# Kernel optimization log

Hardware: AMD Instinct MI355X
Metric: run time of the kernel (lower is better)

The kernel has to match this reference:

```python
import jax, jax.numpy as jnp
import numpy as np

GRID = 16
PAD = 32
RADIUS = 8
SIGMA = 1.5
B = 8192
N_SEEDS = 24


def setup_inputs() -> dict:
    key = jax.random.key(0)
    k1, k2 = jax.random.split(key)
    # predicted seeds: (x, y, phase), coords in [0, GRID)
    output = jax.random.uniform(k1, (B, N_SEEDS * 3), dtype=jnp.float32) * GRID
    # target seeds: (x, y, amp), coords in [0, 2*GRID)
    targets = jax.random.uniform(k2, (B, N_SEEDS * 3), dtype=jnp.float32) * (2 * GRID)
    return {"output": output, "targets": targets}


def _forward(output, targets):
    Bn = output.shape[0]
    seeds = output.reshape(Bn, -1, 3)   # (B, N, 3): x, y, phase
    tgt = targets.reshape(Bn, -1, 3)    # (B, M, 3): x, y, amp

    # --- discrete Voronoi on GRID x GRID (vectorized over batch) ---
    c = jnp.arange(GRID, dtype=output.dtype)
    xx, yy = jnp.meshgrid(c, c, indexing='ij')  # (GRID, GRID)
    dist = jnp.sqrt((xx[None, :, :, None] - seeds[:, None, None, :, 0]) ** 2
                    + (yy[None, :, :, None] - seeds[:, None, None, :, 1]) ** 2)
    labels = jnp.argmin(dist, axis=-1)  # (B, GRID, GRID) int

    # circular support on the inner grid (np.ogrid[-r:r, -r:r] convention)
    cc = jnp.arange(-RADIUS, RADIUS)
    inner = (cc[:, None] ** 2 + cc[None, :] ** 2) <= RADIUS ** 2
    labels = jnp.where(inner[None], labels, 0)

    # zero-pad voronoi labels to PAD x PAD
    pw = (PAD - GRID) // 2
    padded = jnp.pad(labels, ((0, 0), (pw, pw), (pw, pw)))  # (B, PAD, PAD)

    # --- gather phase per pixel, zero outside circle on padded grid ---
    phases = seeds[:, :, 2]  # (B, N)
    phase = jnp.take_along_axis(phases, padded.reshape(Bn, -1), axis=1).reshape(Bn, PAD, PAD)
    pc = jnp.arange(PAD)
    center = PAD // 2
    outside = (pc[:, None] - center) ** 2 + (pc[None, :] - center) ** 2 > RADIUS ** 2
    phase = jnp.where(outside[None], jnp.zeros_like(phase), phase)

    # --- density = amp(=1) * exp(i * 2*pi * phase), shifted FFT magnitude ---
    two_pi = 2.0 * jnp.pi
    density = jax.lax.complex(jnp.cos(two_pi * phase), jnp.sin(two_pi * phase))
    pred = jnp.fft.fftshift(density, axes=(-2, -1))
    pred = jnp.fft.fft2(pred)
    pred_dp = jnp.abs(jnp.fft.fftshift(pred, axes=(-2, -1)))  # (B, PAD, PAD)

    # --- target diffraction: sum of Gaussians on (2*GRID)x(2*GRID) grid ---
    xc = jnp.arange(PAD, dtype=targets.dtype)  # height == width == 2*GRID == PAD
    tx = tgt[:, :, 0][:, :, None, None]
    ty = tgt[:, :, 1][:, :, None, None]
    amp = tgt[:, :, 2][:, :, None, None]
    # torch: x varies along last axis, y along second-to-last
    d2 = (xc[None, None, None, :] - tx) ** 2 + (xc[None, None, :, None] - ty) ** 2
    tgt_dp = jnp.sum(amp * jnp.exp(-d2 / (2.0 * SIGMA ** 2)), axis=1)  # (B, PAD, PAD)

    # --- chi-square (global max-normalization and reductions) ---
    p = pred_dp / jnp.max(pred_dp)
    t = tgt_dp / jnp.max(tgt_dp)
    return jnp.sum((p - t) ** 2) / jnp.sqrt(jnp.sum(p ** 2) * jnp.sum(t ** 2))


def reference(output, targets):
    return _forward(output, targets)
```

## Files before the change

kernel.cpp:

```cpp
#include <hip/hip_runtime.h>
#include <math.h>

#define NS 24

typedef float v2f __attribute__((ext_vector_type(2)));
typedef float v4f __attribute__((ext_vector_type(4)));


struct PixTab { unsigned short v[196]; };
__device__ constexpr PixTab make_pix() {
    PixTab t{};
    int n = 0;
    const int w[16] = {0,3,5,6,6,7,7,7,8,7,7,7,6,6,5,3};
    for (int yy = 0; yy < 16; ++yy)
        for (int x = 16 - w[yy]; x <= 16 + w[yy]; ++x)
            if (x < 24) { t.v[n] = (unsigned short)((yy << 8) | x); n = n + 1; }
    t.v[195] = (unsigned short)((8 << 8) | 24);
    return t;
}
__device__ constexpr PixTab PIX = make_pix();

struct ZTab { unsigned short v[76]; };
__device__ constexpr ZTab make_ztab() {
    ZTab z{};
    bool mark[16][17] = {};
    const int w[16] = {0,3,5,6,6,7,7,7,8,7,7,7,6,6,5,3};
    for (int yy = 0; yy < 16; ++yy)
        for (int x = 16 - w[yy]; x <= 16 + w[yy]; ++x)
            if (x < 24) mark[yy][x - 8] = true;
    mark[8][16] = true;
    int n = 0;
    for (int yy = 0; yy < 16; ++yy)
        for (int xi = 0; xi < 17; ++xi)
            if (!mark[yy][xi]) { z.v[n] = (unsigned short)(yy * 18 + xi); n = n + 1; }
    return z;
}
__device__ constexpr ZTab ZT = make_ztab();

constexpr float twc_(int p) {
    const float C[17] = {
        1.0f, 0.98078528040323044913f, 0.92387953251128675613f, 0.83146961230254523708f,
        0.70710678118654752440f, 0.55557023301960222474f, 0.38268343236508977173f,
        0.19509032201612826785f, 0.0f,
        -0.19509032201612826785f, -0.38268343236508977173f, -0.55557023301960222474f,
        -0.70710678118654752440f, -0.83146961230254523708f, -0.92387953251128675613f,
        -0.98078528040323044913f, -1.0f };
    return (p <= 16) ? C[p] : C[32 - p];
}
constexpr float tws_(int p) {
    const float S[17] = {
        0.0f, 0.19509032201612826785f, 0.38268343236508977173f, 0.55557023301960222474f,
        0.70710678118654752440f, 0.83146961230254523708f, 0.92387953251128675613f,
        0.98078528040323044913f, 1.0f,
        0.98078528040323044913f, 0.92387953251128675613f, 0.83146961230254523708f,
        0.70710678118654752440f, 0.55557023301960222474f, 0.38268343236508977173f,
        0.19509032201612826785f, 0.0f };
    return (p <= 16) ? -S[p] : S[32 - p];
}
struct alignas(16) TW1T { float v[8 * 18 * 2]; };
__device__ constexpr TW1T make_tw1() {
    TW1T t{};
    for (int l0 = 0; l0 < 8; ++l0)
        for (int xi = 0; xi < 17; ++xi) {
            int p = (l0 * (xi + 8)) & 31;
            t.v[(l0 * 18 + xi) * 2 + 0] = twc_(p);
            t.v[(l0 * 18 + xi) * 2 + 1] = tws_(p);
        }
    return t;
}
__device__ constexpr TW1T TW1G = make_tw1();
struct alignas(16) TW2T { float v[4 * 18 * 2]; };
__device__ constexpr TW2T make_tw2() {
    TW2T t{};
    for (int k0 = 0; k0 < 4; ++k0)
        for (int yp = 0; yp < 16; ++yp) {
            int p = (k0 * (yp + 8)) & 31;
            t.v[(k0 * 18 + yp) * 2 + 0] = twc_(p);
            t.v[(k0 * 18 + yp) * 2 + 1] = tws_(p);
        }
    return t;
}
__device__ constexpr TW2T TW2G = make_tw2();

static __device__ __forceinline__ v2f cmul(v2f e, v2f w) {
    v2f m = (v2f){e.y, e.y} * (v2f){w.y, w.x};
    return __builtin_elementwise_fma((v2f){e.x, e.x}, w, (v2f){-m.x, m.y});
}
static __device__ __forceinline__ float mag(v2f h) {
    v2f q = h * h;
    return sqrtf(q.x + q.y);
}

template <int CTRL>
static __device__ __forceinline__ float dpp_step(float x) {
    int y = __builtin_amdgcn_update_dpp(0, __float_as_int(x), CTRL, 0xf, 0xf, true);
    return __int_as_float(y);
}
static __device__ __forceinline__ float wave_sum(float x) {
    x += dpp_step<0x111>(x);
    x += dpp_step<0x112>(x);
    x += dpp_step<0x114>(x);
    x += dpp_step<0x118>(x);
    x += dpp_step<0x142>(x);
    x += dpp_step<0x143>(x);
    return x;
}
static __device__ __forceinline__ float wave_max(float x) {
    x = fmaxf(x, dpp_step<0x111>(x));
    x = fmaxf(x, dpp_step<0x112>(x));
    x = fmaxf(x, dpp_step<0x114>(x));
    x = fmaxf(x, dpp_step<0x118>(x));
    x = fmaxf(x, dpp_step<0x142>(x));
    x = fmaxf(x, dpp_step<0x143>(x));
    return x;
}

__global__ __launch_bounds__(256)
void loss_main(const float* __restrict__ output, const float* __restrict__ targets,
               float* __restrict__ partials, int B) {
    __shared__ float2 e24s;
    __shared__ __align__(16) float gx[NS * 32];
    __shared__ __align__(16) float gyT[32 * 24];
    __shared__ __align__(16) float e2f[16 * 18 * 2];
    __shared__ __align__(16) float tw2f[4 * 36];
    __shared__ __align__(16) float gT2f[32 * 36];
    __shared__ __align__(16) char uA[5120];
    __shared__ float redm[2][5];

    float* tw1f = (float*)uA;
    float* pmf  = (float*)uA;

    const int b = blockIdx.x;
    const int t = threadIdx.x;
    const float* so = output + b * NS * 3;
    const float* tg = targets + b * NS * 3;

    if (t == 0) {
        float sv0, cv0;
        __sincosf(6.2831853071795864f * so[2], &sv0, &cv0);
        e24s = make_float2(cv0 - 1.0f, sv0);
    }
    if (t < 108) {
        if (t < 72) *(v4f*)&tw1f[t * 4] = *(const v4f*)&TW1G.v[t * 4];
        else        *(v4f*)&tw2f[(t - 72) * 4] = *(const v4f*)&TW2G.v[(t - 72) * 4];
    }
    for (int idx = t; idx < NS * 32; idx += 256) {
        int s = idx >> 5, c = idx & 31;
        float dx = (float)c - tg[3 * s];
        gx[idx] = tg[3 * s + 2] * __expf(dx * dx * (-1.0f / 4.5f));
    }
    for (int idx = t; idx < 32 * 24; idx += 256) {
        int r = idx / 24, s = idx - r * 24;
        float dy = (float)r - tg[3 * s + 1];
        gyT[idx] = __expf(dy * dy * (-1.0f / 4.5f));
    }
    if (t < 98) {
        int pv0 = PIX.v[t], pv1 = PIX.v[t + 98];
        int yy0 = pv0 >> 8, x0 = (pv0 & 255) - 8;
        int yy1 = pv1 >> 8, x1 = (pv1 & 255) - 8;
        v2f FI = {(float)yy0, (float)yy1};
        v2f FJ = {(float)x0, (float)x1};
        v2f bd = {1e30f, 1e30f};
        v2f bph = {0.f, 0.f};
#pragma unroll
        for (int s = 0; s < NS; ++s) {
            float sx = so[3 * s], sy = so[3 * s + 1], phs = so[3 * s + 2];
            v2f dX = FI - (v2f){sx, sx};
            v2f dY = FJ - (v2f){sy, sy};
            v2f d2 = __builtin_elementwise_fma(dX, dX, dY * dY);
            if (d2.x < bd.x) { bd.x = d2.x; bph.x = phs; }
            if (d2.y < bd.y) { bd.y = d2.y; bph.y = phs; }
        }
        float ph1 = (t == 97) ? so[2] : bph.y;
        float sv0, cv0, sv1, cv1;
        __sincosf(6.2831853071795864f * bph.x, &sv0, &cv0);
        __sincosf(6.2831853071795864f * ph1, &sv1, &cv1);
        *(v2f*)&e2f[(yy0 * 18 + x0) * 2] = (v2f){cv0 - 1.0f, sv0};
        *(v2f*)&e2f[(yy1 * 18 + x1) * 2] = (v2f){cv1 - 1.0f, sv1};
    } else if (t < 98 + 76) {
        int idx = (int)ZT.v[t - 98];
        *(v2f*)&e2f[idx * 2] = (v2f){0.f, 0.f};
    }
    __syncthreads();

    v2f ta01 = {0,0}, ta23 = {0,0}, tb01 = {0,0}, tb23 = {0,0};

    if (t < 128) {
        int yy = t >> 3, l0 = t & 7;
        const float* row = &e2f[yy * 36];
        const float* twr = &tw1f[l0 * 36];
        v2f c0 = {0,0}, c1 = {0,0}, c2 = {0,0}, c3 = {0,0};
#pragma unroll
        for (int q = 0; q < 8; ++q) {
            v4f e4 = *(const v4f*)&row[q * 4];
            v4f w4 = *(const v4f*)&twr[q * 4];
            v2f ca = cmul((v2f){e4.x, e4.y}, (v2f){w4.x, w4.y});
            v2f cb = cmul((v2f){e4.z, e4.w}, (v2f){w4.z, w4.w});
            if ((q & 1) == 0) { c0 += ca; c1 += cb; }
            else              { c2 += ca; c3 += cb; }
        }
        {
            v2f e16 = *(const v2f*)&row[32];
            v2f w16 = *(const v2f*)&twr[32];
            c0 += cmul(e16, w16);
        }
        v2f a = c0 + c2, bb = c0 - c2;
        v2f cc = c1 + c3, d = c1 - c3;
        v2f du = {d.y, -d.x};
        *(v2f*)&gT2f[l0 * 36 + yy * 2]        = a + cc;
        *(v2f*)&gT2f[(l0 + 8) * 36 + yy * 2]  = bb + du;
        *(v2f*)&gT2f[(l0 + 16) * 36 + yy * 2] = a - cc;
        *(v2f*)&gT2f[(l0 + 24) * 36 + yy * 2] = bb - du;
    } else {
        int tid2 = t - 128;
        int r = tid2 >> 3;
        int c0i = (tid2 & 7) * 4;
#pragma unroll
        for (int q = 0; q < 6; ++q) {
            v4f gy4a = *(const v4f*)&gyT[r * 24 + q * 4];
            v4f gy4b = *(const v4f*)&gyT[(r + 16) * 24 + q * 4];
#pragma unroll
            for (int j = 0; j < 4; ++j) {
                v4f g4 = *(const v4f*)&gx[(4 * q + j) * 32 + c0i];
                float ga = (j == 0) ? gy4a.x : (j == 1) ? gy4a.y : (j == 2) ? gy4a.z : gy4a.w;
                float gb = (j == 0) ? gy4b.x : (j == 1) ? gy4b.y : (j == 2) ? gy4b.z : gy4b.w;
                v2f glo = {g4.x, g4.y}, ghi = {g4.z, g4.w};
                ta01 = __builtin_elementwise_fma((v2f){ga, ga}, glo, ta01);
                ta23 = __builtin_elementwise_fma((v2f){ga, ga}, ghi, ta23);
                tb01 = __builtin_elementwise_fma((v2f){gb, gb}, glo, tb01);
                tb23 = __builtin_elementwise_fma((v2f){gb, gb}, ghi, tb23);
            }
        }
    }
    __syncthreads();

    if (t < 128) {
        int l = t >> 2, k0 = t & 3;
        const float* gTr = &gT2f[l * 36];
        const float* twr = &tw2f[k0 * 36];
        v2f c[8];
#pragma unroll
        for (int q = 0; q < 4; ++q) {
            v4f glo = *(const v4f*)&gTr[q * 4];
            v4f ghi = *(const v4f*)&gTr[q * 4 + 16];
            v4f wlo = *(const v4f*)&twr[q * 4];
            v4f whi = *(const v4f*)&twr[q * 4 + 16];
            c[2 * q]     = cmul((v2f){glo.x, glo.y}, (v2f){wlo.x, wlo.y})
                         + cmul((v2f){ghi.x, ghi.y}, (v2f){whi.x, whi.y});
            c[2 * q + 1] = cmul((v2f){glo.z, glo.w}, (v2f){wlo.z, wlo.w})
                         + cmul((v2f){ghi.z, ghi.w}, (v2f){whi.z, whi.w});
        }
        v2f Ea = c[0] + c[4], Eb = c[0] - c[4];
        v2f Ec = c[2] + c[6], Ed = c[2] - c[6];
        v2f Edu = {Ed.y, -Ed.x};
        v2f E0 = Ea + Ec, E1 = Eb + Edu, E2 = Ea - Ec, E3 = Eb - Edu;
        v2f Oa = c[1] + c[5], Ob = c[1] - c[5];
        v2f Oc = c[3] + c[7], Od = c[3] - c[7];
        v2f Odu = {Od.y, -Od.x};
        v2f O0 = Oa + Oc, O1 = Ob + Odu, O2 = Oa - Oc, O3 = Ob - Odu;
        const float s2 = 0.70710678118654752440f;
        v2f w1O = (v2f){s2, s2} * (v2f){O1.x + O1.y, O1.y - O1.x};
        v2f w3O = (v2f){s2, s2} * (v2f){O3.y - O3.x, -(O3.x + O3.y)};
        v2f miO = {O2.y, -O2.x};
        {
            float2 e24 = e24s;
            float ar2 = (k0 == 0) ? 1.f : (k0 == 2) ? -1.f : 0.f;
            float ai2 = (k0 == 1) ? 1.f : (k0 == 3) ? -1.f : 0.f;
            float sgn = (l & 1) ? -1.f : 1.f;
            v2f T = {sgn * (e24.x * ar2 - e24.y * ai2),
                     sgn * (e24.x * ai2 + e24.y * ar2)};
            E0 += T; E1 += T; E2 += T; E3 += T;
        }
        v2f h0 = E0 + O0;
        if (t == 0) h0.x += 1024.0f;
        int v = (l + 16) & 31;
        pmf[(k0 + 16) * 40 + v] = mag(h0);
        pmf[(k0 + 20) * 40 + v] = mag(E1 + w1O);
        pmf[(k0 + 24) * 40 + v] = mag(E2 + miO);
        pmf[(k0 + 28) * 40 + v] = mag(E3 + w3O);
        pmf[(k0)      * 40 + v] = mag(E0 - O0);
        pmf[(k0 + 4)  * 40 + v] = mag(E1 - w1O);
        pmf[(k0 + 8)  * 40 + v] = mag(E2 - miO);
        pmf[(k0 + 12) * 40 + v] = mag(E3 - w3O);
    }
    __syncthreads();

    if (t >= 128) {
        int tid2 = t - 128;
        int r = tid2 >> 3;
        int c0i = (tid2 & 7) * 4;
        v4f p4a = *(const v4f*)&pmf[r * 40 + c0i];
        v4f p4b = *(const v4f*)&pmf[(r + 16) * 40 + c0i];
        v2f pa01 = {p4a.x, p4a.y}, pa23 = {p4a.z, p4a.w};
        v2f pb01 = {p4b.x, p4b.y}, pb23 = {p4b.z, p4b.w};
        v2f s2v = pa01 * pa01 + pa23 * pa23 + pb01 * pb01 + pb23 * pb23;
        v2f t2v = ta01 * ta01 + ta23 * ta23 + tb01 * tb01 + tb23 * tb23;
        v2f ptv = pa01 * ta01 + pa23 * ta23 + pb01 * tb01 + pb23 * tb23;
        float sp2 = s2v.x + s2v.y;
        float st2 = t2v.x + t2v.y;
        float spt = ptv.x + ptv.y;
        float mp = fmaxf(fmaxf(fmaxf(p4a.x, p4a.y), fmaxf(p4a.z, p4a.w)),
                         fmaxf(fmaxf(p4b.x, p4b.y), fmaxf(p4b.z, p4b.w)));
        v2f tm = __builtin_elementwise_max(__builtin_elementwise_max(ta01, ta23),
                                           __builtin_elementwise_max(tb01, tb23));
        float mt = fmaxf(tm.x, tm.y);
        sp2 = wave_sum(sp2);
        st2 = wave_sum(st2);
        spt = wave_sum(spt);
        mp  = wave_max(mp);
        mt  = wave_max(mt);
        int wv = (t >> 6) - 2, lane = t & 63;
        if (lane == 63) {
            redm[wv][0] = sp2; redm[wv][1] = st2; redm[wv][2] = spt;
            redm[wv][3] = mp;  redm[wv][4] = mt;
        }
    }
    __syncthreads();
    if (t == 0) {
        partials[0 * B + b] = redm[0][0] + redm[1][0];
        partials[1 * B + b] = redm[0][1] + redm[1][1];
        partials[2 * B + b] = redm[0][2] + redm[1][2];
        partials[3 * B + b] = fmaxf(redm[0][3], redm[1][3]);
        partials[4 * B + b] = fmaxf(redm[0][4], redm[1][4]);
    }
}

__global__ __launch_bounds__(1024)
void finalize_loss(const float* __restrict__ partials, float* __restrict__ out, int B) {
    __shared__ double reds[16][3];
    __shared__ float redx[16][2];
    const int t = threadIdx.x;
    double sp2 = 0.0, st2 = 0.0, spt = 0.0;
    float mp = 0.f, mt = 0.f;
    for (int i = t; i < B; i += 1024) {
        sp2 += (double)partials[0 * B + i];
        st2 += (double)partials[1 * B + i];
        spt += (double)partials[2 * B + i];
        mp = fmaxf(mp, partials[3 * B + i]);
        mt = fmaxf(mt, partials[4 * B + i]);
    }
    for (int off = 32; off > 0; off >>= 1) {
        sp2 += __shfl_down(sp2, off);
        st2 += __shfl_down(st2, off);
        spt += __shfl_down(spt, off);
        mp = fmaxf(mp, __shfl_down(mp, off));
        mt = fmaxf(mt, __shfl_down(mt, off));
    }
    int wave = t >> 6, lane = t & 63;
    if (lane == 0) {
        reds[wave][0] = sp2; reds[wave][1] = st2; reds[wave][2] = spt;
        redx[wave][0] = mp;  redx[wave][1] = mt;
    }
    __syncthreads();
    if (t == 0) {
        for (int w = 1; w < 16; ++w) {
            sp2 += reds[w][0];
            st2 += reds[w][1];
            spt += reds[w][2];
            mp = fmaxf(mp, redx[w][0]);
            mt = fmaxf(mt, redx[w][1]);
        }
        double Mp = (double)mp, Mt = (double)mt;
        double loss = (sp2 * (Mt / Mp) + st2 * (Mp / Mt) - 2.0 * spt) / sqrt(sp2 * st2);
        out[0] = (float)loss;
    }
}

extern "C" void kernel_launch(void* const* d_in, const int* in_sizes, int n_in,
                              void* d_out, int out_size, void* d_ws, size_t ws_size,
                              hipStream_t stream) {
    const float* output  = (const float*)d_in[0];
    const float* targets = (const float*)d_in[1];
    int B = in_sizes[0] / (NS * 3);
    float* partials = (float*)d_ws;

    loss_main<<<B, 256, 0, stream>>>(output, targets, partials, B);
    finalize_loss<<<1, 1024, 0, stream>>>(partials, (float*)d_out, B);
}
```

Before: 94.77 us.

## Map one wavefront per batch element and replace block barriers with wave barriers

Each 256-thread block now handles four batch elements, one per 64-lane wave, instead of one element spread across four waves. Each wave gets private LDS regions for the Gaussian tables, the FFT buffers and the magnitudes. It does the Voronoi, both FFT passes, the target sum and the reductions itself, so `__syncthreads` becomes `wave_barrier` and the cross-wave reduction step goes away. The aim is to cut block-level sync and idle-wave overhead, in exchange for more serial work per wave and a larger LDS footprint per block (about 40 KB), which may limit how many blocks fit on a CU. The pixel table is padded to 256 entries so every lane takes four pixels, and the zero-fill table is replaced by a plain clear of the buffer.

```diff
diff --git a/kernel.cpp b/kernel.cpp
--- a/kernel.cpp
+++ b/kernel.cpp
@@ -7,7 +7,7 @@
 typedef float v4f __attribute__((ext_vector_type(4)));
 
 
-struct PixTab { unsigned short v[196]; };
+struct PixTab { unsigned short v[256]; };
 __device__ constexpr PixTab make_pix() {
     PixTab t{};
     int n = 0;
@@ -16,26 +16,11 @@
         for (int x = 16 - w[yy]; x <= 16 + w[yy]; ++x)
             if (x < 24) { t.v[n] = (unsigned short)((yy << 8) | x); n = n + 1; }
     t.v[195] = (unsigned short)((8 << 8) | 24);
+    for (int e = 196; e < 256; ++e)
+        t.v[e] = (unsigned short)(((e & 15) << 8) | 25);
     return t;
 }
 __device__ constexpr PixTab PIX = make_pix();
-
-struct ZTab { unsigned short v[76]; };
-__device__ constexpr ZTab make_ztab() {
-    ZTab z{};
-    bool mark[16][17] = {};
-    const int w[16] = {0,3,5,6,6,7,7,7,8,7,7,7,6,6,5,3};
-    for (int yy = 0; yy < 16; ++yy)
-        for (int x = 16 - w[yy]; x <= 16 + w[yy]; ++x)
-            if (x < 24) mark[yy][x - 8] = true;
-    mark[8][16] = true;
-    int n = 0;
-    for (int yy = 0; yy < 16; ++yy)
-        for (int xi = 0; xi < 17; ++xi)
-            if (!mark[yy][xi]) { z.v[n] = (unsigned short)(yy * 18 + xi); n = n + 1; }
-    return z;
-}
-__device__ constexpr ZTab ZT = make_ztab();
 
 constexpr float twc_(int p) {
     const float C[17] = {
@@ -115,78 +100,130 @@
     return x;
 }
 
-__global__ __launch_bounds__(256)
+__global__ __launch_bounds__(256, 4)
 void loss_main(const float* __restrict__ output, const float* __restrict__ targets,
-               float* __restrict__ partials, int B) {
-    __shared__ float2 e24s;
-    __shared__ __align__(16) float gx[NS * 32];
-    __shared__ __align__(16) float gyT[32 * 24];
-    __shared__ __align__(16) float e2f[16 * 18 * 2];
-    __shared__ __align__(16) float tw2f[4 * 36];
-    __shared__ __align__(16) float gT2f[32 * 36];
-    __shared__ __align__(16) char uA[5120];
-    __shared__ float redm[2][5];
-
-    float* tw1f = (float*)uA;
-    float* pmf  = (float*)uA;
-
-    const int b = blockIdx.x;
+               float* __restrict__ partials, int Btot) {
+    __shared__ __align__(16) char lds_all[40640];
+    float* tw1f = (float*)lds_all;
+    float* tw2f = (float*)(lds_all + 1152);
     const int t = threadIdx.x;
-    const float* so = output + b * NS * 3;
-    const float* tg = targets + b * NS * 3;
-
-    if (t == 0) {
-        float sv0, cv0;
-        __sincosf(6.2831853071795864f * so[2], &sv0, &cv0);
-        e24s = make_float2(cv0 - 1.0f, sv0);
-    }
-    if (t < 108) {
-        if (t < 72) *(v4f*)&tw1f[t * 4] = *(const v4f*)&TW1G.v[t * 4];
-        else        *(v4f*)&tw2f[(t - 72) * 4] = *(const v4f*)&TW2G.v[(t - 72) * 4];
-    }
-    for (int idx = t; idx < NS * 32; idx += 256) {
+    const int lane = t & 63;
+    const int w = __builtin_amdgcn_readfirstlane(t >> 6);
+    char* wbase = lds_all + 1728 + w * 9728;
+    float* R1 = (float*)wbase;
+    float* R2 = (float*)(wbase + 5120);
+    const int batch = blockIdx.x * 4 + w;
+    if (batch >= Btot) return;
+    const float* so = output + batch * (NS * 3);
+    const float* tg = targets + batch * (NS * 3);
+    const float TP = 6.2831853071795864f;
+
+    {
+        int i0 = lane;
+        *(v4f*)&tw1f[i0 * 4] = *(const v4f*)&TW1G.v[i0 * 4];
+        int i1 = lane + 64;
+        if (i1 < 72)       *(v4f*)&tw1f[i1 * 4] = *(const v4f*)&TW1G.v[i1 * 4];
+        else if (i1 < 108) *(v4f*)&tw2f[(i1 - 72) * 4] = *(const v4f*)&TW2G.v[(i1 - 72) * 4];
+    }
+
+    float* gx  = R1;
+    float* gyT = R2;
+#pragma unroll
+    for (int k = 0; k < 12; ++k) {
+        int idx = lane + 64 * k;
         int s = idx >> 5, c = idx & 31;
         float dx = (float)c - tg[3 * s];
         gx[idx] = tg[3 * s + 2] * __expf(dx * dx * (-1.0f / 4.5f));
     }
-    for (int idx = t; idx < 32 * 24; idx += 256) {
+#pragma unroll
+    for (int k = 0; k < 12; ++k) {
+        int idx = lane + 64 * k;
         int r = idx / 24, s = idx - r * 24;
         float dy = (float)r - tg[3 * s + 1];
-        gyT[idx] = __expf(dy * dy * (-1.0f / 4.5f));
-    }
-    if (t < 98) {
-        int pv0 = PIX.v[t], pv1 = PIX.v[t + 98];
-        int yy0 = pv0 >> 8, x0 = (pv0 & 255) - 8;
-        int yy1 = pv1 >> 8, x1 = (pv1 & 255) - 8;
-        v2f FI = {(float)yy0, (float)yy1};
-        v2f FJ = {(float)x0, (float)x1};
-        v2f bd = {1e30f, 1e30f};
-        v2f bph = {0.f, 0.f};
+        gyT[r * 28 + s] = __expf(dy * dy * (-1.0f / 4.5f));
+    }
+    __builtin_amdgcn_wave_barrier();
+
+    const int rr = lane >> 2;
+    const int cc0 = (lane & 3) * 8;
+    v2f ta0 = {0,0}, ta1 = {0,0}, ta2 = {0,0}, ta3 = {0,0};
+    v2f tb0 = {0,0}, tb1 = {0,0}, tb2 = {0,0}, tb3 = {0,0};
+#pragma unroll
+    for (int q = 0; q < 6; ++q) {
+        v4f gy4a = *(const v4f*)&gyT[rr * 28 + q * 4];
+        v4f gy4b = *(const v4f*)&gyT[(rr + 16) * 28 + q * 4];
+#pragma unroll
+        for (int j = 0; j < 4; ++j) {
+            v4f glo = *(const v4f*)&gx[(4 * q + j) * 32 + cc0];
+            v4f ghi = *(const v4f*)&gx[(4 * q + j) * 32 + cc0 + 4];
+            float ga = (j == 0) ? gy4a.x : (j == 1) ? gy4a.y : (j == 2) ? gy4a.z : gy4a.w;
+            float gb = (j == 0) ? gy4b.x : (j == 1) ? gy4b.y : (j == 2) ? gy4b.z : gy4b.w;
+            v2f g01 = {glo.x, glo.y}, g23 = {glo.z, glo.w};
+            v2f g45 = {ghi.x, ghi.y}, g67 = {ghi.z, ghi.w};
+            ta0 = __builtin_elementwise_fma((v2f){ga, ga}, g01, ta0);
+            ta1 = __builtin_elementwise_fma((v2f){ga, ga}, g23, ta1);
+            ta2 = __builtin_elementwise_fma((v2f){ga, ga}, g45, ta2);
+            ta3 = __builtin_elementwise_fma((v2f){ga, ga}, g67, ta3);
+            tb0 = __builtin_elementwise_fma((v2f){gb, gb}, g01, tb0);
+            tb1 = __builtin_elementwise_fma((v2f){gb, gb}, g23, tb1);
+            tb2 = __builtin_elementwise_fma((v2f){gb, gb}, g45, tb2);
+            tb3 = __builtin_elementwise_fma((v2f){gb, gb}, g67, tb3);
+        }
+    }
+    __builtin_amdgcn_wave_barrier();
+
+    float* e2f = R1;
+#pragma unroll
+    for (int o = 0; o < 3; ++o) {
+        int idx = lane + 64 * o;
+        if (idx < 144) *(v4f*)&e2f[idx * 4] = (v4f){0.f, 0.f, 0.f, 0.f};
+    }
+
+    {
+        unsigned ppA = *(const unsigned*)&PIX.v[2 * lane];
+        unsigned ppB = *(const unsigned*)&PIX.v[2 * lane + 128];
+        int pvA0 = (int)(ppA & 0xffffu), pvA1 = (int)(ppA >> 16);
+        int pvB0 = (int)(ppB & 0xffffu), pvB1 = (int)(ppB >> 16);
+        int yA0 = pvA0 >> 8, xA0 = (pvA0 & 255) - 8;
+        int yA1 = pvA1 >> 8, xA1 = (pvA1 & 255) - 8;
+        int yB0 = pvB0 >> 8, xB0 = (pvB0 & 255) - 8;
+        int yB1 = pvB1 >> 8, xB1 = (pvB1 & 255) - 8;
+        v2f FIA = {(float)yA0, (float)yA1}, FJA = {(float)xA0, (float)xA1};
+        v2f FIB = {(float)yB0, (float)yB1}, FJB = {(float)xB0, (float)xB1};
+        v2f bdA = {1e30f, 1e30f}, bphA = {0.f, 0.f};
+        v2f bdB = {1e30f, 1e30f}, bphB = {0.f, 0.f};
 #pragma unroll
         for (int s = 0; s < NS; ++s) {
             float sx = so[3 * s], sy = so[3 * s + 1], phs = so[3 * s + 2];
-            v2f dX = FI - (v2f){sx, sx};
-            v2f dY = FJ - (v2f){sy, sy};
-            v2f d2 = __builtin_elementwise_fma(dX, dX, dY * dY);
-            if (d2.x < bd.x) { bd.x = d2.x; bph.x = phs; }
-            if (d2.y < bd.y) { bd.y = d2.y; bph.y = phs; }
-        }
-        float ph1 = (t == 97) ? so[2] : bph.y;
-        float sv0, cv0, sv1, cv1;
-        __sincosf(6.2831853071795864f * bph.x, &sv0, &cv0);
-        __sincosf(6.2831853071795864f * ph1, &sv1, &cv1);
-        *(v2f*)&e2f[(yy0 * 18 + x0) * 2] = (v2f){cv0 - 1.0f, sv0};
-        *(v2f*)&e2f[(yy1 * 18 + x1) * 2] = (v2f){cv1 - 1.0f, sv1};
-    } else if (t < 98 + 76) {
-        int idx = (int)ZT.v[t - 98];
-        *(v2f*)&e2f[idx * 2] = (v2f){0.f, 0.f};
-    }
-    __syncthreads();
-
-    v2f ta01 = {0,0}, ta23 = {0,0}, tb01 = {0,0}, tb23 = {0,0};
-
-    if (t < 128) {
-        int yy = t >> 3, l0 = t & 7;
+            v2f dXA = FIA - (v2f){sx, sx};
+            v2f dYA = FJA - (v2f){sy, sy};
+            v2f d2A = __builtin_elementwise_fma(dXA, dXA, dYA * dYA);
+            v2f dXB = FIB - (v2f){sx, sx};
+            v2f dYB = FJB - (v2f){sy, sy};
+            v2f d2B = __builtin_elementwise_fma(dXB, dXB, dYB * dYB);
+            if (d2A.x < bdA.x) { bdA.x = d2A.x; bphA.x = phs; }
+            if (d2A.y < bdA.y) { bdA.y = d2A.y; bphA.y = phs; }
+            if (d2B.x < bdB.x) { bdB.x = d2B.x; bphB.x = phs; }
+            if (d2B.y < bdB.y) { bdB.y = d2B.y; bphB.y = phs; }
+        }
+        float phB1 = (2 * lane + 129 == 195) ? so[2] : bphB.y;
+        float svA0, cvA0, svA1, cvA1, svB0, cvB0, svB1, cvB1;
+        __sincosf(TP * bphA.x, &svA0, &cvA0);
+        __sincosf(TP * bphA.y, &svA1, &cvA1);
+        __sincosf(TP * bphB.x, &svB0, &cvB0);
+        __sincosf(TP * phB1,   &svB1, &cvB1);
+        *(v2f*)&e2f[(yA0 * 18 + xA0) * 2] = (v2f){cvA0 - 1.0f, svA0};
+        *(v2f*)&e2f[(yA1 * 18 + xA1) * 2] = (v2f){cvA1 - 1.0f, svA1};
+        *(v2f*)&e2f[(yB0 * 18 + xB0) * 2] = (v2f){cvB0 - 1.0f, svB0};
+        *(v2f*)&e2f[(yB1 * 18 + xB1) * 2] = (v2f){cvB1 - 1.0f, svB1};
+    }
+    __builtin_amdgcn_wave_barrier();
+
+    float* gT2f = R2;
+#pragma unroll
+    for (int h = 0; h < 2; ++h) {
+        const int tau = lane + 64 * h;
+        const int yy = tau >> 3, l0 = tau & 7;
         const float* row = &e2f[yy * 36];
         const float* twr = &tw1f[l0 * 36];
         v2f c0 = {0,0}, c1 = {0,0}, c2 = {0,0}, c3 = {0,0};
@@ -211,31 +248,17 @@
         *(v2f*)&gT2f[(l0 + 8) * 36 + yy * 2]  = bb + du;
         *(v2f*)&gT2f[(l0 + 16) * 36 + yy * 2] = a - cc;
         *(v2f*)&gT2f[(l0 + 24) * 36 + yy * 2] = bb - du;
-    } else {
-        int tid2 = t - 128;
-        int r = tid2 >> 3;
-        int c0i = (tid2 & 7) * 4;
-#pragma unroll
-        for (int q = 0; q < 6; ++q) {
-            v4f gy4a = *(const v4f*)&gyT[r * 24 + q * 4];
-            v4f gy4b = *(const v4f*)&gyT[(r + 16) * 24 + q * 4];
-#pragma unroll
-            for (int j = 0; j < 4; ++j) {
-                v4f g4 = *(const v4f*)&gx[(4 * q + j) * 32 + c0i];
-                float ga = (j == 0) ? gy4a.x : (j == 1) ? gy4a.y : (j == 2) ? gy4a.z : gy4a.w;
-                float gb = (j == 0) ? gy4b.x : (j == 1) ? gy4b.y : (j == 2) ? gy4b.z : gy4b.w;
-                v2f glo = {g4.x, g4.y}, ghi = {g4.z, g4.w};
-                ta01 = __builtin_elementwise_fma((v2f){ga, ga}, glo, ta01);
-                ta23 = __builtin_elementwise_fma((v2f){ga, ga}, ghi, ta23);
-                tb01 = __builtin_elementwise_fma((v2f){gb, gb}, glo, tb01);
-                tb23 = __builtin_elementwise_fma((v2f){gb, gb}, ghi, tb23);
-            }
-        }
-    }
-    __syncthreads();
-
-    if (t < 128) {
-        int l = t >> 2, k0 = t & 3;
+    }
+    __builtin_amdgcn_wave_barrier();
+
+    float sv24, cv24;
+    __sincosf(TP * so[2], &sv24, &cv24);
+    const float e24x = cv24 - 1.0f, e24y = sv24;
+    float* pmf = R1;
+#pragma unroll
+    for (int h = 0; h < 2; ++h) {
+        const int tau = lane + 64 * h;
+        const int l = tau >> 2, k0 = tau & 3;
         const float* gTr = &gT2f[l * 36];
         const float* twr = &tw2f[k0 * 36];
         v2f c[8];
@@ -258,21 +281,20 @@
         v2f Oc = c[3] + c[7], Od = c[3] - c[7];
         v2f Odu = {Od.y, -Od.x};
         v2f O0 = Oa + Oc, O1 = Ob + Odu, O2 = Oa - Oc, O3 = Ob - Odu;
-        const float s2 = 0.70710678118654752440f;
-        v2f w1O = (v2f){s2, s2} * (v2f){O1.x + O1.y, O1.y - O1.x};
-        v2f w3O = (v2f){s2, s2} * (v2f){O3.y - O3.x, -(O3.x + O3.y)};
+        const float s2c = 0.70710678118654752440f;
+        v2f w1O = (v2f){s2c, s2c} * (v2f){O1.x + O1.y, O1.y - O1.x};
+        v2f w3O = (v2f){s2c, s2c} * (v2f){O3.y - O3.x, -(O3.x + O3.y)};
         v2f miO = {O2.y, -O2.x};
         {
-            float2 e24 = e24s;
             float ar2 = (k0 == 0) ? 1.f : (k0 == 2) ? -1.f : 0.f;
             float ai2 = (k0 == 1) ? 1.f : (k0 == 3) ? -1.f : 0.f;
             float sgn = (l & 1) ? -1.f : 1.f;
-            v2f T = {sgn * (e24.x * ar2 - e24.y * ai2),
-                     sgn * (e24.x * ai2 + e24.y * ar2)};
+            v2f T = {sgn * (e24x * ar2 - e24y * ai2),
+                     sgn * (e24x * ai2 + e24y * ar2)};
             E0 += T; E1 += T; E2 += T; E3 += T;
         }
         v2f h0 = E0 + O0;
-        if (t == 0) h0.x += 1024.0f;
+        if (tau == 0) h0.x += 1024.0f;
         int v = (l + 16) & 31;
         pmf[(k0 + 16) * 40 + v] = mag(h0);
         pmf[(k0 + 20) * 40 + v] = mag(E1 + w1O);
@@ -283,45 +305,47 @@
         pmf[(k0 + 8)  * 40 + v] = mag(E2 - miO);
         pmf[(k0 + 12) * 40 + v] = mag(E3 - w3O);
     }
-    __syncthreads();
-
-    if (t >= 128) {
-        int tid2 = t - 128;
-        int r = tid2 >> 3;
-        int c0i = (tid2 & 7) * 4;
-        v4f p4a = *(const v4f*)&pmf[r * 40 + c0i];
-        v4f p4b = *(const v4f*)&pmf[(r + 16) * 40 + c0i];
-        v2f pa01 = {p4a.x, p4a.y}, pa23 = {p4a.z, p4a.w};
-        v2f pb01 = {p4b.x, p4b.y}, pb23 = {p4b.z, p4b.w};
-        v2f s2v = pa01 * pa01 + pa23 * pa23 + pb01 * pb01 + pb23 * pb23;
-        v2f t2v = ta01 * ta01 + ta23 * ta23 + tb01 * tb01 + tb23 * tb23;
-        v2f ptv = pa01 * ta01 + pa23 * ta23 + pb01 * tb01 + pb23 * tb23;
+    __builtin_amdgcn_wave_barrier();
+
+    {
+        v4f p4a = *(const v4f*)&pmf[rr * 40 + cc0];
+        v4f p4b = *(const v4f*)&pmf[rr * 40 + cc0 + 4];
+        v4f p4c = *(const v4f*)&pmf[(rr + 16) * 40 + cc0];
+        v4f p4d = *(const v4f*)&pmf[(rr + 16) * 40 + cc0 + 4];
+        v2f pa0 = {p4a.x, p4a.y}, pa1 = {p4a.z, p4a.w};
+        v2f pa2 = {p4b.x, p4b.y}, pa3 = {p4b.z, p4b.w};
+        v2f pb0 = {p4c.x, p4c.y}, pb1 = {p4c.z, p4c.w};
+        v2f pb2 = {p4d.x, p4d.y}, pb3 = {p4d.z, p4d.w};
+        v2f s2v = pa0 * pa0 + pa1 * pa1 + pa2 * pa2 + pa3 * pa3
+                + pb0 * pb0 + pb1 * pb1 + pb2 * pb2 + pb3 * pb3;
+        v2f t2v = ta0 * ta0 + ta1 * ta1 + ta2 * ta2 + ta3 * ta3
+                + tb0 * tb0 + tb1 * tb1 + tb2 * tb2 + tb3 * tb3;
+        v2f ptv = pa0 * ta0 + pa1 * ta1 + pa2 * ta2 + pa3 * ta3
+                + pb0 * tb0 + pb1 * tb1 + pb2 * tb2 + pb3 * tb3;
         float sp2 = s2v.x + s2v.y;
         float st2 = t2v.x + t2v.y;
         float spt = ptv.x + ptv.y;
-        float mp = fmaxf(fmaxf(fmaxf(p4a.x, p4a.y), fmaxf(p4a.z, p4a.w)),
-                         fmaxf(fmaxf(p4b.x, p4b.y), fmaxf(p4b.z, p4b.w)));
-        v2f tm = __builtin_elementwise_max(__builtin_elementwise_max(ta01, ta23),
-                                           __builtin_elementwise_max(tb01, tb23));
-        float mt = fmaxf(tm.x, tm.y);
+        v4f pmx = __builtin_elementwise_max(__builtin_elementwise_max(p4a, p4b),
+                                            __builtin_elementwise_max(p4c, p4d));
+        float mp = fmaxf(fmaxf(pmx.x, pmx.y), fmaxf(pmx.z, pmx.w));
+        v2f tmx = __builtin_elementwise_max(__builtin_elementwise_max(ta0, ta1),
+                                            __builtin_elementwise_max(ta2, ta3));
+        tmx = __builtin_elementwise_max(tmx,
+              __builtin_elementwise_max(__builtin_elementwise_max(tb0, tb1),
+                                        __builtin_elementwise_max(tb2, tb3)));
+        float mt = fmaxf(tmx.x, tmx.y);
         sp2 = wave_sum(sp2);
         st2 = wave_sum(st2);
         spt = wave_sum(spt);
         mp  = wave_max(mp);
         mt  = wave_max(mt);
-        int wv = (t >> 6) - 2, lane = t & 63;
         if (lane == 63) {
-            redm[wv][0] = sp2; redm[wv][1] = st2; redm[wv][2] = spt;
-            redm[wv][3] = mp;  redm[wv][4] = mt;
-        }
-    }
-    __syncthreads();
-    if (t == 0) {
-        partials[0 * B + b] = redm[0][0] + redm[1][0];
-        partials[1 * B + b] = redm[0][1] + redm[1][1];
-        partials[2 * B + b] = redm[0][2] + redm[1][2];
-        partials[3 * B + b] = fmaxf(redm[0][3], redm[1][3]);
-        partials[4 * B + b] = fmaxf(redm[0][4], redm[1][4]);
+            partials[0 * Btot + batch] = sp2;
+            partials[1 * Btot + batch] = st2;
+            partials[2 * Btot + batch] = spt;
+            partials[3 * Btot + batch] = mp;
+            partials[4 * Btot + batch] = mt;
+        }
     }
 }
 
@@ -374,6 +398,7 @@
     int B = in_sizes[0] / (NS * 3);
     float* partials = (float*)d_ws;
 
-    loss_main<<<B, 256, 0, stream>>>(output, targets, partials, B);
+    int nb = (B + 3) >> 2;
+    loss_main<<<nb, 256, 0, stream>>>(output, targets, partials, B);
     finalize_loss<<<1, 1024, 0, stream>>>(partials, (float*)d_out, B);
 }
```

Measured after the change: 166.2 us. +75.4%, slower.

## Fuse final reduction into main kernel via last-block atomic counter

Applied to the files above, without the earlier changes.

Removes the separate finalize kernel: each block bumps a global atomic counter after writing its partials, and the last block to finish does the cross-block reduction and writes the loss. Shared memory is also repacked so that gx, tw1f and e2f live in one union buffer, which lowers the per-block LDS footprint and may allow more blocks per CU. The trade-off is a memset launch for the counter, a threadfence and an atomic in every block, and a serial tail reduction done by a single 256-thread block.

```diff
diff --git a/kernel.cpp b/kernel.cpp
--- a/kernel.cpp
+++ b/kernel.cpp
@@ -117,17 +117,21 @@
 
 __global__ __launch_bounds__(256)
 void loss_main(const float* __restrict__ output, const float* __restrict__ targets,
-               float* __restrict__ partials, int B) {
+               float* __restrict__ partials, float* __restrict__ out,
+               int* __restrict__ counter, int B) {
     __shared__ float2 e24s;
-    __shared__ __align__(16) float gx[NS * 32];
+    __shared__ __align__(16) char uA[6528];
     __shared__ __align__(16) float gyT[32 * 24];
-    __shared__ __align__(16) float e2f[16 * 18 * 2];
     __shared__ __align__(16) float tw2f[4 * 36];
     __shared__ __align__(16) float gT2f[32 * 36];
-    __shared__ __align__(16) char uA[5120];
     __shared__ float redm[2][5];
-
-    float* tw1f = (float*)uA;
+    __shared__ double redd[4][3];
+    __shared__ float redf[4][2];
+    __shared__ int lastFlag;
+
+    float* gx   = (float*)uA;
+    float* tw1f = (float*)(uA + 3072);
+    float* e2f  = (float*)(uA + 4224);
     float* pmf  = (float*)uA;
 
     const int b = blockIdx.x;
@@ -322,47 +326,49 @@
         partials[2 * B + b] = redm[0][2] + redm[1][2];
         partials[3 * B + b] = fmaxf(redm[0][3], redm[1][3]);
         partials[4 * B + b] = fmaxf(redm[0][4], redm[1][4]);
-    }
-}
-
-__global__ __launch_bounds__(1024)
-void finalize_loss(const float* __restrict__ partials, float* __restrict__ out, int B) {
-    __shared__ double reds[16][3];
-    __shared__ float redx[16][2];
-    const int t = threadIdx.x;
-    double sp2 = 0.0, st2 = 0.0, spt = 0.0;
-    float mp = 0.f, mt = 0.f;
-    for (int i = t; i < B; i += 1024) {
-        sp2 += (double)partials[0 * B + i];
-        st2 += (double)partials[1 * B + i];
-        spt += (double)partials[2 * B + i];
-        mp = fmaxf(mp, partials[3 * B + i]);
-        mt = fmaxf(mt, partials[4 * B + i]);
-    }
-    for (int off = 32; off > 0; off >>= 1) {
-        sp2 += __shfl_down(sp2, off);
-        st2 += __shfl_down(st2, off);
-        spt += __shfl_down(spt, off);
-        mp = fmaxf(mp, __shfl_down(mp, off));
-        mt = fmaxf(mt, __shfl_down(mt, off));
-    }
-    int wave = t >> 6, lane = t & 63;
-    if (lane == 0) {
-        reds[wave][0] = sp2; reds[wave][1] = st2; reds[wave][2] = spt;
-        redx[wave][0] = mp;  redx[wave][1] = mt;
-    }
-    __syncthreads();
-    if (t == 0) {
-        for (int w = 1; w < 16; ++w) {
-            sp2 += reds[w][0];
-            st2 += reds[w][1];
-            spt += reds[w][2];
-            mp = fmaxf(mp, redx[w][0]);
-            mt = fmaxf(mt, redx[w][1]);
-        }
-        double Mp = (double)mp, Mt = (double)mt;
-        double loss = (sp2 * (Mt / Mp) + st2 * (Mp / Mt) - 2.0 * spt) / sqrt(sp2 * st2);
-        out[0] = (float)loss;
+        __threadfence();
+        int tk = atomicAdd(counter, 1);
+        lastFlag = (tk == (int)gridDim.x - 1);
+    }
+    __syncthreads();
+    if (!lastFlag) return;
+
+    __threadfence();
+    {
+        double sp2 = 0.0, st2 = 0.0, spt = 0.0;
+        float mp = 0.f, mt = 0.f;
+        for (int i = t; i < B; i += 256) {
+            sp2 += (double)partials[0 * B + i];
+            st2 += (double)partials[1 * B + i];
+            spt += (double)partials[2 * B + i];
+            mp = fmaxf(mp, partials[3 * B + i]);
+            mt = fmaxf(mt, partials[4 * B + i]);
+        }
+        for (int off = 32; off > 0; off >>= 1) {
+            sp2 += __shfl_down(sp2, off);
+            st2 += __shfl_down(st2, off);
+            spt += __shfl_down(spt, off);
+            mp = fmaxf(mp, __shfl_down(mp, off));
+            mt = fmaxf(mt, __shfl_down(mt, off));
+        }
+        int wv = t >> 6, lane = t & 63;
+        if (lane == 0) {
+            redd[wv][0] = sp2; redd[wv][1] = st2; redd[wv][2] = spt;
+            redf[wv][0] = mp;  redf[wv][1] = mt;
+        }
+        __syncthreads();
+        if (t == 0) {
+            for (int w = 1; w < 4; ++w) {
+                sp2 += redd[w][0];
+                st2 += redd[w][1];
+                spt += redd[w][2];
+                mp = fmaxf(mp, redf[w][0]);
+                mt = fmaxf(mt, redf[w][1]);
+            }
+            double Mp = (double)mp, Mt = (double)mt;
+            double loss = (sp2 * (Mt / Mp) + st2 * (Mp / Mt) - 2.0 * spt) / sqrt(sp2 * st2);
+            out[0] = (float)loss;
+        }
     }
 }
 
@@ -373,7 +379,9 @@
     const float* targets = (const float*)d_in[1];
     int B = in_sizes[0] / (NS * 3);
     float* partials = (float*)d_ws;
-
-    loss_main<<<B, 256, 0, stream>>>(output, targets, partials, B);
-    finalize_loss<<<1, 1024, 0, stream>>>(partials, (float*)d_out, B);
-}
+    int* counter = (int*)((char*)d_ws + 5 * B * sizeof(float));
+
+    hipMemsetAsync(counter, 0, sizeof(int), stream);
+    loss_main<<<B, 256, 0, stream>>>(output, targets, partials, (float*)d_out,
+                                     counter, B);
+}
```

Result: slower. 248.8 us (+162.6%).

## Remap FFT stages per wave to drop a block barrier; spread Voronoi over 196 threads

Applied to the files above, without the earlier changes.

The Voronoi labelling now uses one pixel per thread across 196 threads instead of two pixels per thread across 98, and the zero-fill work moves to the remaining threads. The row and column FFT stages are remapped so each 64-lane wave produces exactly the gT2f rows it later consumes. This lets a wave barrier replace one block-wide __syncthreads between the two FFT stages. tw1f and pmf get their own shared buffers instead of aliasing one region, which raises LDS use per block and could lower occupancy.

```diff
diff --git a/kernel.cpp b/kernel.cpp
--- a/kernel.cpp
+++ b/kernel.cpp
@@ -122,13 +122,11 @@
     __shared__ __align__(16) float gx[NS * 32];
     __shared__ __align__(16) float gyT[32 * 24];
     __shared__ __align__(16) float e2f[16 * 18 * 2];
+    __shared__ __align__(16) float tw1f[8 * 36];
     __shared__ __align__(16) float tw2f[4 * 36];
     __shared__ __align__(16) float gT2f[32 * 36];
-    __shared__ __align__(16) char uA[5120];
+    __shared__ __align__(16) float pmf[32 * 40];
     __shared__ float redm[2][5];
-
-    float* tw1f = (float*)uA;
-    float* pmf  = (float*)uA;
 
     const int b = blockIdx.x;
     const int t = threadIdx.x;
@@ -154,63 +152,116 @@
         float dy = (float)r - tg[3 * s + 1];
         gyT[idx] = __expf(dy * dy * (-1.0f / 4.5f));
     }
-    if (t < 98) {
-        int pv0 = PIX.v[t], pv1 = PIX.v[t + 98];
-        int yy0 = pv0 >> 8, x0 = (pv0 & 255) - 8;
-        int yy1 = pv1 >> 8, x1 = (pv1 & 255) - 8;
-        v2f FI = {(float)yy0, (float)yy1};
-        v2f FJ = {(float)x0, (float)x1};
-        v2f bd = {1e30f, 1e30f};
-        v2f bph = {0.f, 0.f};
+    if (t < 196) {
+        int pv = PIX.v[t];
+        int yy = pv >> 8, x = (pv & 255) - 8;
+        float fi = (float)yy, fj = (float)x;
+        float bd = 1e30f, bph = 0.f;
 #pragma unroll
         for (int s = 0; s < NS; ++s) {
             float sx = so[3 * s], sy = so[3 * s + 1], phs = so[3 * s + 2];
-            v2f dX = FI - (v2f){sx, sx};
-            v2f dY = FJ - (v2f){sy, sy};
-            v2f d2 = __builtin_elementwise_fma(dX, dX, dY * dY);
-            if (d2.x < bd.x) { bd.x = d2.x; bph.x = phs; }
-            if (d2.y < bd.y) { bd.y = d2.y; bph.y = phs; }
-        }
-        float ph1 = (t == 97) ? so[2] : bph.y;
-        float sv0, cv0, sv1, cv1;
-        __sincosf(6.2831853071795864f * bph.x, &sv0, &cv0);
-        __sincosf(6.2831853071795864f * ph1, &sv1, &cv1);
-        *(v2f*)&e2f[(yy0 * 18 + x0) * 2] = (v2f){cv0 - 1.0f, sv0};
-        *(v2f*)&e2f[(yy1 * 18 + x1) * 2] = (v2f){cv1 - 1.0f, sv1};
-    } else if (t < 98 + 76) {
-        int idx = (int)ZT.v[t - 98];
-        *(v2f*)&e2f[idx * 2] = (v2f){0.f, 0.f};
+            float dX = fi - sx;
+            float dY = fj - sy;
+            float d2 = __builtin_fmaf(dX, dX, dY * dY);
+            if (d2 < bd) { bd = d2; bph = phs; }
+        }
+        float ph = (t == 195) ? so[2] : bph;
+        float sv0, cv0;
+        __sincosf(6.2831853071795864f * ph, &sv0, &cv0);
+        *(v2f*)&e2f[(yy * 18 + x) * 2] = (v2f){cv0 - 1.0f, sv0};
+    } else {
+        int idx0 = t - 196;
+        *(v2f*)&e2f[(int)ZT.v[idx0] * 2] = (v2f){0.f, 0.f};
+        if (idx0 < 16)
+            *(v2f*)&e2f[(int)ZT.v[idx0 + 60] * 2] = (v2f){0.f, 0.f};
     }
     __syncthreads();
 
     v2f ta01 = {0,0}, ta23 = {0,0}, tb01 = {0,0}, tb23 = {0,0};
 
     if (t < 128) {
-        int yy = t >> 3, l0 = t & 7;
-        const float* row = &e2f[yy * 36];
-        const float* twr = &tw1f[l0 * 36];
-        v2f c0 = {0,0}, c1 = {0,0}, c2 = {0,0}, c3 = {0,0};
-#pragma unroll
-        for (int q = 0; q < 8; ++q) {
-            v4f e4 = *(const v4f*)&row[q * 4];
-            v4f w4 = *(const v4f*)&twr[q * 4];
-            v2f ca = cmul((v2f){e4.x, e4.y}, (v2f){w4.x, w4.y});
-            v2f cb = cmul((v2f){e4.z, e4.w}, (v2f){w4.z, w4.w});
-            if ((q & 1) == 0) { c0 += ca; c1 += cb; }
-            else              { c2 += ca; c3 += cb; }
-        }
         {
-            v2f e16 = *(const v2f*)&row[32];
-            v2f w16 = *(const v2f*)&twr[32];
-            c0 += cmul(e16, w16);
-        }
-        v2f a = c0 + c2, bb = c0 - c2;
-        v2f cc = c1 + c3, d = c1 - c3;
-        v2f du = {d.y, -d.x};
-        *(v2f*)&gT2f[l0 * 36 + yy * 2]        = a + cc;
-        *(v2f*)&gT2f[(l0 + 8) * 36 + yy * 2]  = bb + du;
-        *(v2f*)&gT2f[(l0 + 16) * 36 + yy * 2] = a - cc;
-        *(v2f*)&gT2f[(l0 + 24) * 36 + yy * 2] = bb - du;
+            int l0 = t >> 4, yy = t & 15;
+            const float* row = &e2f[yy * 36];
+            const float* twr = &tw1f[l0 * 36];
+            v2f c0 = {0,0}, c1 = {0,0}, c2 = {0,0}, c3 = {0,0};
+#pragma unroll
+            for (int q = 0; q < 8; ++q) {
+                v4f e4 = *(const v4f*)&row[q * 4];
+                v4f w4 = *(const v4f*)&twr[q * 4];
+                v2f ca = cmul((v2f){e4.x, e4.y}, (v2f){w4.x, w4.y});
+                v2f cb = cmul((v2f){e4.z, e4.w}, (v2f){w4.z, w4.w});
+                if ((q & 1) == 0) { c0 += ca; c1 += cb; }
+                else              { c2 += ca; c3 += cb; }
+            }
+            {
+                v2f e16 = *(const v2f*)&row[32];
+                v2f w16 = *(const v2f*)&twr[32];
+                c0 += cmul(e16, w16);
+            }
+            v2f a = c0 + c2, bb = c0 - c2;
+            v2f cc = c1 + c3, d = c1 - c3;
+            v2f du = {d.y, -d.x};
+            *(v2f*)&gT2f[l0 * 36 + yy * 2]        = a + cc;
+            *(v2f*)&gT2f[(l0 + 8) * 36 + yy * 2]  = bb + du;
+            *(v2f*)&gT2f[(l0 + 16) * 36 + yy * 2] = a - cc;
+            *(v2f*)&gT2f[(l0 + 24) * 36 + yy * 2] = bb - du;
+        }
+        __builtin_amdgcn_wave_barrier();
+
+        {
+            int base = (t >= 64) ? 4 : 0;
+            int idx = t & 63;
+            int lsel = idx >> 2;
+            int l = base + (lsel & 3) + 8 * (lsel >> 2);
+            int k0 = idx & 3;
+            const float* gTr = &gT2f[l * 36];
+            const float* twr = &tw2f[k0 * 36];
+            v2f c[8];
+#pragma unroll
+            for (int q = 0; q < 4; ++q) {
+                v4f glo = *(const v4f*)&gTr[q * 4];
+                v4f ghi = *(const v4f*)&gTr[q * 4 + 16];
+                v4f wlo = *(const v4f*)&twr[q * 4];
+                v4f whi = *(const v4f*)&twr[q * 4 + 16];
+                c[2 * q]     = cmul((v2f){glo.x, glo.y}, (v2f){wlo.x, wlo.y})
+                             + cmul((v2f){ghi.x, ghi.y}, (v2f){whi.x, whi.y});
+                c[2 * q + 1] = cmul((v2f){glo.z, glo.w}, (v2f){wlo.z, wlo.w})
+                             + cmul((v2f){ghi.z, ghi.w}, (v2f){whi.z, whi.w});
+            }
+            v2f Ea = c[0] + c[4], Eb = c[0] - c[4];
+            v2f Ec = c[2] + c[6], Ed = c[2] - c[6];
+            v2f Edu = {Ed.y, -Ed.x};
+            v2f E0 = Ea + Ec, E1 = Eb + Edu, E2 = Ea - Ec, E3 = Eb - Edu;
+            v2f Oa = c[1] + c[5], Ob = c[1] - c[5];
+            v2f Oc = c[3] + c[7], Od = c[3] - c[7];
+            v2f Odu = {Od.y, -Od.x};
+            v2f O0 = Oa + Oc, O1 = Ob + Odu, O2 = Oa - Oc, O3 = Ob - Odu;
+            const float s2 = 0.70710678118654752440f;
+            v2f w1O = (v2f){s2, s2} * (v2f){O1.x + O1.y, O1.y - O1.x};
+            v2f w3O = (v2f){s2, s2} * (v2f){O3.y - O3.x, -(O3.x + O3.y)};
+            v2f miO = {O2.y, -O2.x};
+            {
+                float2 e24 = e24s;
+                float ar2 = (k0 == 0) ? 1.f : (k0 == 2) ? -1.f : 0.f;
+                float ai2 = (k0 == 1) ? 1.f : (k0 == 3) ? -1.f : 0.f;
+                float sgn = (l & 1) ? -1.f : 1.f;
+                v2f T = {sgn * (e24.x * ar2 - e24.y * ai2),
+                         sgn * (e24.x * ai2 + e24.y * ar2)};
+                E0 += T; E1 += T; E2 += T; E3 += T;
+            }
+            v2f h0 = E0 + O0;
+            if ((l | k0) == 0) h0.x += 1024.0f;
+            int v = (l + 16) & 31;
+            pmf[(k0 + 16) * 40 + v] = mag(h0);
+            pmf[(k0 + 20) * 40 + v] = mag(E1 + w1O);
+            pmf[(k0 + 24) * 40 + v] = mag(E2 + miO);
+            pmf[(k0 + 28) * 40 + v] = mag(E3 + w3O);
+            pmf[(k0)      * 40 + v] = mag(E0 - O0);
+            pmf[(k0 + 4)  * 40 + v] = mag(E1 - w1O);
+            pmf[(k0 + 8)  * 40 + v] = mag(E2 - miO);
+            pmf[(k0 + 12) * 40 + v] = mag(E3 - w3O);
+        }
     } else {
         int tid2 = t - 128;
         int r = tid2 >> 3;
@@ -231,57 +282,6 @@
                 tb23 = __builtin_elementwise_fma((v2f){gb, gb}, ghi, tb23);
             }
         }
-    }
-    __syncthreads();
-
-    if (t < 128) {
-        int l = t >> 2, k0 = t & 3;
-        const float* gTr = &gT2f[l * 36];
-        const float* twr = &tw2f[k0 * 36];
-        v2f c[8];
-#pragma unroll
-        for (int q = 0; q < 4; ++q) {
-            v4f glo = *(const v4f*)&gTr[q * 4];
-            v4f ghi = *(const v4f*)&gTr[q * 4 + 16];
-            v4f wlo = *(const v4f*)&twr[q * 4];
-            v4f whi = *(const v4f*)&twr[q * 4 + 16];
-            c[2 * q]     = cmul((v2f){glo.x, glo.y}, (v2f){wlo.x, wlo.y})
-                         + cmul((v2f){ghi.x, ghi.y}, (v2f){whi.x, whi.y});
-            c[2 * q + 1] = cmul((v2f){glo.z, glo.w}, (v2f){wlo.z, wlo.w})
-                         + cmul((v2f){ghi.z, ghi.w}, (v2f){whi.z, whi.w});
-        }
-        v2f Ea = c[0] + c[4], Eb = c[0] - c[4];
-        v2f Ec = c[2] + c[6], Ed = c[2] - c[6];
-        v2f Edu = {Ed.y, -Ed.x};
-        v2f E0 = Ea + Ec, E1 = Eb + Edu, E2 = Ea - Ec, E3 = Eb - Edu;
-        v2f Oa = c[1] + c[5], Ob = c[1] - c[5];
-        v2f Oc = c[3] + c[7], Od = c[3] - c[7];
-        v2f Odu = {Od.y, -Od.x};
-        v2f O0 = Oa + Oc, O1 = Ob + Odu, O2 = Oa - Oc, O3 = Ob - Odu;
-        const float s2 = 0.70710678118654752440f;
-        v2f w1O = (v2f){s2, s2} * (v2f){O1.x + O1.y, O1.y - O1.x};
-        v2f w3O = (v2f){s2, s2} * (v2f){O3.y - O3.x, -(O3.x + O3.y)};
-        v2f miO = {O2.y, -O2.x};
-        {
-            float2 e24 = e24s;
-            float ar2 = (k0 == 0) ? 1.f : (k0 == 2) ? -1.f : 0.f;
-            float ai2 = (k0 == 1) ? 1.f : (k0 == 3) ? -1.f : 0.f;
-            float sgn = (l & 1) ? -1.f : 1.f;
-            v2f T = {sgn * (e24.x * ar2 - e24.y * ai2),
-                     sgn * (e24.x * ai2 + e24.y * ar2)};
-            E0 += T; E1 += T; E2 += T; E3 += T;
-        }
-        v2f h0 = E0 + O0;
-        if (t == 0) h0.x += 1024.0f;
-        int v = (l + 16) & 31;
-        pmf[(k0 + 16) * 40 + v] = mag(h0);
-        pmf[(k0 + 20) * 40 + v] = mag(E1 + w1O);
-        pmf[(k0 + 24) * 40 + v] = mag(E2 + miO);
-        pmf[(k0 + 28) * 40 + v] = mag(E3 + w3O);
-        pmf[(k0)      * 40 + v] = mag(E0 - O0);
-        pmf[(k0 + 4)  * 40 + v] = mag(E1 - w1O);
-        pmf[(k0 + 8)  * 40 + v] = mag(E2 - miO);
-        pmf[(k0 + 12) * 40 + v] = mag(E3 - w3O);
     }
     __syncthreads();
 
```

Result: no change. 94.62 us (-0.2%).
